# Optimization experiments

Hardware: AMD Instinct MI355X
Metric: run time of the kernel (lower is better)

The kernel has to match this reference:

```python
import jax, jax.numpy as jnp
import numpy as np

NUM_GRAPHS = 16


def gat_layer(x, src, dst, n, W, a_s, a_d, b):
    # PyG GATConv, concat=False (mean over heads), negative_slope=0.2
    H, C = a_s.shape
    h = (x @ W).reshape(x.shape[0], H, C)            # [N,H,C]
    es = jnp.einsum('nhc,hc->nh', h, a_s)            # alpha_src per node
    ed = jnp.einsum('nhc,hc->nh', h, a_d)            # alpha_dst per node
    e = jax.nn.leaky_relu(es[src] + ed[dst], 0.2)    # [E,H]
    m = jax.ops.segment_max(e, dst, num_segments=n)
    m = jnp.where(jnp.isfinite(m), m, 0.0)
    p = jnp.exp(e - m[dst])
    denom = jax.ops.segment_sum(p, dst, num_segments=n)
    alpha = p / (denom[dst] + 1e-16)                 # segment softmax over in-edges
    out = jax.ops.segment_sum(h[src] * alpha[..., None], dst, num_segments=n)  # [N,H,C]
    return out.mean(axis=1) + b


def _forward(x, edge_index, batch,
             W_e0, a_s_e0, a_d_e0, b_e0, W_e1, a_s_e1, a_d_e1, b_e1,
             W_d0, a_s_d0, a_d_d0, b_d0, W_d1, a_s_d1, a_d_d1, b_d1,
             g_w1, g_b1, g_w2, g_b2):
    n = x.shape[0]
    loop = jnp.arange(n, dtype=edge_index.dtype)     # PyG add_self_loops=True
    src = jnp.concatenate([edge_index[0], loop])
    dst = jnp.concatenate([edge_index[1], loop])
    # encoder (dropout inert in eval)
    h = jax.nn.relu(gat_layer(x, src, dst, n, W_e0, a_s_e0, a_d_e0, b_e0))
    h = gat_layer(h, src, dst, n, W_e1, a_s_e1, a_d_e1, b_e1)
    # GlobalAttention pooling: gate MLP -> segment softmax over graphs -> scatter sum
    gate = (jax.nn.relu(h @ g_w1 + g_b1) @ g_w2 + g_b2)[:, 0]   # [N]
    gm = jax.ops.segment_max(gate, batch, num_segments=NUM_GRAPHS)
    gm = jnp.where(jnp.isfinite(gm), gm, 0.0)
    p = jnp.exp(gate - gm[batch])
    att = p / (jax.ops.segment_sum(p, batch, num_segments=NUM_GRAPHS)[batch] + 1e-16)
    pooled = jax.ops.segment_sum(att[:, None] * h, batch, num_segments=NUM_GRAPHS)
    h = pooled[batch]                                # broadcast pooled back to nodes
    # decoder (heads=1)
    h = jax.nn.relu(gat_layer(h, src, dst, n, W_d0, a_s_d0, a_d_d0, b_d0))
    return gat_layer(h, src, dst, n, W_d1, a_s_d1, a_d_d1, b_d1)


def setup_inputs() -> dict:
    key = jax.random.key(0)
    ks = jax.random.split(key, 24)
    N, E, Din, H, C = 50000, 250000, 128, 8, 64
    def w(k, shape, fan_in):
        return (jax.random.normal(k, shape, jnp.float32) / np.sqrt(fan_in)).astype(jnp.float32)
    return {
        'x': jax.random.normal(ks[0], (N, Din), jnp.float32),
        'edge_index': jax.random.randint(ks[1], (2, E), 0, N, dtype=jnp.int32),
        'batch': jnp.sort(jax.random.randint(ks[2], (N,), 0, NUM_GRAPHS, dtype=jnp.int32)),
        'W_e0': w(ks[3], (Din, H * C), Din), 'a_s_e0': w(ks[4], (H, C), C), 'a_d_e0': w(ks[5], (H, C), C), 'b_e0': w(ks[6], (C,), C),
        'W_e1': w(ks[7], (C, H * C), C), 'a_s_e1': w(ks[8], (H, C), C), 'a_d_e1': w(ks[9], (H, C), C), 'b_e1': w(ks[10], (C,), C),
        'W_d0': w(ks[11], (C, C), C), 'a_s_d0': w(ks[12], (1, C), C), 'a_d_d0': w(ks[13], (1, C), C), 'b_d0': w(ks[14], (C,), C),
        'W_d1': w(ks[15], (C, Din), C), 'a_s_d1': w(ks[16], (1, Din), Din), 'a_d_d1': w(ks[17], (1, Din), Din), 'b_d1': w(ks[18], (Din,), Din),
        'g_w1': w(ks[19], (C, C), C), 'g_b1': w(ks[20], (C,), C), 'g_w2': w(ks[21], (C, 1), C), 'g_b2': w(ks[22], (1,), C),
    }


def reference(x, edge_index, batch,
              W_e0, a_s_e0, a_d_e0, b_e0, W_e1, a_s_e1, a_d_e1, b_e1,
              W_d0, a_s_d0, a_d_d0, b_d0, W_d1, a_s_d1, a_d_d1, b_d1,
              g_w1, g_b1, g_w2, g_b2):
    return _forward(x, edge_index, batch,
                    W_e0, a_s_e0, a_d_e0, b_e0, W_e1, a_s_e1, a_d_e1, b_e1,
                    W_d0, a_s_d0, a_d_d0, b_d0, W_d1, a_s_d1, a_d_d1, b_d1,
                    g_w1, g_b1, g_w2, g_b2)
```

## Files before the change

kernel.cpp:

```cpp
#include <hip/hip_runtime.h>
#include <hip/hip_fp16.h>
#include <math.h>

#define TB 256

typedef _Float16 half8v __attribute__((ext_vector_type(8)));
typedef float float4v __attribute__((ext_vector_type(4)));

static __device__ __forceinline__ int edge_src(const int* ei, int E, int e) {
    return (e < E) ? ei[e] : (e - E);
}
static __device__ __forceinline__ int edge_dst(const int* ei, int E, int e) {
    return (e < E) ? ei[E + e] : (e - E);
}

__global__ void csr_count(const int* __restrict__ ei, int E, int Etot, int* __restrict__ cnt) {
    int e = blockIdx.x * blockDim.x + threadIdx.x;
    if (e >= Etot) return;
    atomicAdd(&cnt[edge_dst(ei, E, e)], 1);
}

__global__ __launch_bounds__(256) void scan_phase1(const int* __restrict__ cnt,
                                                   int* __restrict__ incl,
                                                   int* __restrict__ bsum, int n) {
    __shared__ int sdata[256];
    int t = threadIdx.x;
    int base = blockIdx.x * 256;
    int v = (base + t < n) ? cnt[base + t] : 0;
    for (int d = 1; d < 256; d <<= 1) {
        sdata[t] = v; __syncthreads();
        if (t >= d) v += sdata[t - d];
        __syncthreads();
    }
    if (base + t < n) incl[base + t] = v;
    if (t == 255) bsum[blockIdx.x] = v;
}

__global__ void scan_phase2(int* bsum, int nb) {
    __shared__ int sdata[256];
    int t = threadIdx.x;
    int v = (t < nb) ? bsum[t] : 0;
    for (int d = 1; d < 256; d <<= 1) {
        sdata[t] = v; __syncthreads();
        if (t >= d) v += sdata[t - d];
        __syncthreads();
    }
    if (t < nb) bsum[t] = v;
}

__global__ __launch_bounds__(256) void scan_phase3(const int* __restrict__ incl,
                                                   const int* __restrict__ bsum,
                                                   int* __restrict__ off, int n) {
    int i = blockIdx.x * 256 + threadIdx.x;
    if (i < n) off[i + 1] = incl[i] + (blockIdx.x ? bsum[blockIdx.x - 1] : 0);
    if (i == 0) off[0] = 0;
}

__global__ void csr_fill(const int* __restrict__ ei, int E, int Etot,
                         const int* __restrict__ off, int* __restrict__ cur,
                         int* __restrict__ esrc) {
    int e = blockIdx.x * blockDim.x + threadIdx.x;
    if (e >= Etot) return;
    int d = edge_dst(ei, E, e);
    int pos = atomicAdd(&cur[d], 1);
    esrc[off[d] + pos] = edge_src(ei, E, e);
}

__global__ void find_gstart(const int* __restrict__ batch, int* __restrict__ gstart, int N) {
    int n = blockIdx.x * blockDim.x + threadIdx.x;
    if (n >= N) return;
    int b = batch[n];
    int prev = n ? batch[n - 1] : -1;
    for (int g = prev + 1; g <= b; ++g) gstart[g] = n;
    if (n == N - 1)
        for (int g = b + 1; g <= 16; ++g) gstart[g] = N;
}

__global__ void cast_f2h(const float* __restrict__ in, __half* __restrict__ out, int n) {
    int i2 = (blockIdx.x * blockDim.x + threadIdx.x) * 2;
    if (i2 + 1 < n) {
        float2 v = *(const float2*)(in + i2);
        *(__half2*)(out + i2) = __floats2half2_rn(v.x, v.y);
    } else if (i2 < n) {
        out[i2] = __float2half(in[i2]);
    }
}

__global__ void make_ws(const float* __restrict__ W, const float* __restrict__ a_s,
                        const float* __restrict__ a_d, float* __restrict__ ws,
                        float* __restrict__ wd, int K, int H, int C) {
    int i = blockIdx.x * blockDim.x + threadIdx.x;
    if (i >= H * K) return;
    int h = i / K, k = i % K;
    const float* wrow = W + (size_t)k * H * C + h * C;
    float s = 0.f, d = 0.f;
    for (int c = 0; c < C; ++c) {
        s += wrow[c] * a_s[h * C + c];
        d += wrow[c] * a_d[h * C + c];
    }
    ws[i] = s;
    wd[i] = d;
}

__global__ void transpose_cast(const float* __restrict__ W, __half* __restrict__ WT,
                               int K, int N) {
    int i = blockIdx.x * blockDim.x + threadIdx.x;
    if (i >= N * K) return;
    int nn = i / K, kk = i % K;
    WT[i] = __float2half(W[kk * N + nn]);
}

__global__ void make_wstackT(const float* __restrict__ W, __half* __restrict__ WT,
                             int K, int H, int C) {
    int i = blockIdx.x * blockDim.x + threadIdx.x;
    if (i >= K * H * C) return;
    int c = i / (H * K);
    int rem = i % (H * K);
    int h = rem / K, k = rem % K;
    WT[i] = __float2half(W[(size_t)k * H * C + h * C + c]);
}

template <int K>
__global__ __launch_bounds__(256) void gemm_mfma(const __half* __restrict__ A,
                                                 const __half* __restrict__ BT,
                                                 __half* __restrict__ C,
                                                 int M, int N) {
    constexpr int KP = K + 8;
    __shared__ __align__(16) __half As[64 * KP];
    __shared__ __align__(16) __half Bs[64 * KP];
    int tid = threadIdx.x;
    int bm = blockIdx.y * 64, bn = blockIdx.x * 64;
    constexpr int LPR = K / 8;
    for (int idx = tid; idx < 64 * LPR; idx += 256) {
        int row = idx / LPR, koff = (idx % LPR) * 8;
        uint4 v = make_uint4(0u, 0u, 0u, 0u);
        int gr = bm + row;
        if (gr < M) v = *(const uint4*)(A + (size_t)gr * K + koff);
        *(uint4*)(&As[row * KP + koff]) = v;
        uint4 wv = *(const uint4*)(BT + (size_t)(bn + row) * K + koff);
        *(uint4*)(&Bs[row * KP + koff]) = wv;
    }
    __syncthreads();
    int wv_ = tid >> 6, l = tid & 63;
    int lr = l & 15, g = l >> 4;
    float4v acc[4] = {{0.f, 0.f, 0.f, 0.f}, {0.f, 0.f, 0.f, 0.f},
                      {0.f, 0.f, 0.f, 0.f}, {0.f, 0.f, 0.f, 0.f}};
    const __half* ap = &As[(16 * wv_ + lr) * KP + 8 * g];
    const __half* bp = &Bs[lr * KP + 8 * g];
#pragma unroll
    for (int k0 = 0; k0 < K; k0 += 32) {
        half8v af = *reinterpret_cast<const half8v*>(ap + k0);
#pragma unroll
        for (int nt = 0; nt < 4; ++nt) {
            half8v bf = *reinterpret_cast<const half8v*>(bp + nt * 16 * KP + k0);
            acc[nt] = __builtin_amdgcn_mfma_f32_16x16x32_f16(af, bf, acc[nt], 0, 0, 0);
        }
    }
#pragma unroll
    for (int nt = 0; nt < 4; ++nt) {
#pragma unroll
        for (int r = 0; r < 4; ++r) {
            int grow = bm + 16 * wv_ + 4 * g + r;
            if (grow < M)
                C[(size_t)grow * N + bn + nt * 16 + lr] = __float2half(acc[nt][r]);
        }
    }
}

template <int K, int H>
__global__ __launch_bounds__(256) void scores_nt(const __half* __restrict__ A,
                                                 const float* __restrict__ ws,
                                                 const float* __restrict__ wd,
                                                 float* __restrict__ es,
                                                 float* __restrict__ ed, int N) {
    int n = blockIdx.x * blockDim.x + threadIdx.x;
    if (n >= N) return;
    const __half* row = A + (size_t)n * K;
    float s[H] = {}, d[H] = {};
#pragma unroll
    for (int k0 = 0; k0 < K; k0 += 8) {
        uint4 raw = *(const uint4*)(row + k0);
        const __half* hv = (const __half*)&raw;
        float a[8];
#pragma unroll
        for (int q = 0; q < 8; ++q) a[q] = __half2float(hv[q]);
#pragma unroll
        for (int h = 0; h < H; ++h)
#pragma unroll
            for (int q = 0; q < 8; ++q) {
                s[h] += a[q] * ws[h * K + k0 + q];
                d[h] += a[q] * wd[h * K + k0 + q];
            }
    }
#pragma unroll
    for (int h = 0; h < H; ++h) {
        es[(size_t)n * H + h] = s[h];
        ed[(size_t)n * H + h] = d[h];
    }
}

template <bool RELU>
__global__ __launch_bounds__(256) void gat_gather_h8(const __half* __restrict__ hsrc,
                                                     const float* __restrict__ es,
                                                     const float* __restrict__ ed,
                                                     const int* __restrict__ off,
                                                     const int* __restrict__ esrc,
                                                     const float* __restrict__ bias,
                                                     __half* __restrict__ out, int N) {
    constexpr int HC = 512;
    int n = (blockIdx.x * blockDim.x + threadIdx.x) >> 6;
    int lane = threadIdx.x & 63;
    if (n >= N) return;
    int hd = lane >> 3;
    int k8 = lane >> 3, h8 = lane & 7;
    int j0 = off[n], j1 = off[n + 1];

    float edl = ed[(size_t)n * 8 + h8];

    float acc[8] = {};
    float denacc = 0.f;
    for (int j = j0; j < j1; j += 8) {
        int jj = j + k8;
        int jc = (jj < j1) ? jj : (j1 - 1);
        int sidx = esrc[jc];
        float v = es[(size_t)sidx * 8 + h8] + edl;
        v = (v > 0.f) ? v : 0.2f * v;
        float pm = (jj < j1) ? expf(v) : 0.f;
        denacc += pm;
        uint4 rw[8];
#pragma unroll
        for (int k = 0; k < 8; ++k) {
            int sb = __shfl(sidx, k * 8);
            rw[k] = *(const uint4*)(hsrc + (size_t)sb * HC + 8 * lane);
        }
#pragma unroll
        for (int k = 0; k < 8; ++k) {
            float a = __shfl(pm, k * 8 + hd);
            const __half* hv = (const __half*)&rw[k];
#pragma unroll
            for (int q = 0; q < 8; ++q) acc[q] += a * __half2float(hv[q]);
        }
    }

    float den = denacc;
#pragma unroll
    for (int o = 8; o < 64; o <<= 1) den += __shfl_xor(den, o);
    float dv = __shfl(den, hd) + 1e-16f;

#pragma unroll
    for (int q = 0; q < 8; ++q) acc[q] /= dv;
#pragma unroll
    for (int o = 8; o < 64; o <<= 1)
#pragma unroll
        for (int q = 0; q < 8; ++q) acc[q] += __shfl_xor(acc[q], o);

    if (lane < 8) {
        int cbase = 8 * lane;
        float r[8];
#pragma unroll
        for (int q = 0; q < 8; ++q) {
            float o2 = acc[q] * 0.125f + bias[cbase + q];
            if (RELU) o2 = fmaxf(o2, 0.f);
            r[q] = o2;
        }
        __half2 p0 = __floats2half2_rn(r[0], r[1]);
        __half2 p1 = __floats2half2_rn(r[2], r[3]);
        __half2 p2 = __floats2half2_rn(r[4], r[5]);
        __half2 p3 = __floats2half2_rn(r[6], r[7]);
        uint4 pk;
        pk.x = *(unsigned*)&p0; pk.y = *(unsigned*)&p1;
        pk.z = *(unsigned*)&p2; pk.w = *(unsigned*)&p3;
        *(uint4*)(out + (size_t)n * 64 + cbase) = pk;
    }
}

__global__ __launch_bounds__(256) void gat_gather_z8(const __half* __restrict__ A,
                                                     const float* __restrict__ es,
                                                     const float* __restrict__ ed,
                                                     const int* __restrict__ off,
                                                     const int* __restrict__ esrc,
                                                     __half* __restrict__ z, int N) {
    int n = (blockIdx.x * blockDim.x + threadIdx.x) >> 6;
    int lane = threadIdx.x & 63;
    if (n >= N) return;
    int k8 = lane >> 3, q8 = lane & 7;
    int j0 = off[n], j1 = off[n + 1];
    float edv = ed[n];

    float acc[8] = {};
    float denacc = 0.f;
    for (int j = j0; j < j1; j += 8) {
        int jj = j + k8;
        int jc = (jj < j1) ? jj : (j1 - 1);
        int sidx = esrc[jc];
        float v = es[sidx] + edv;
        v = (v > 0.f) ? v : 0.2f * v;
        float pm = (jj < j1) ? expf(v) : 0.f;
        denacc += pm;
        uint4 rw = *(const uint4*)(A + (size_t)sidx * 64 + 8 * q8);
        const __half* hv = (const __half*)&rw;
#pragma unroll
        for (int q = 0; q < 8; ++q) acc[q] += pm * __half2float(hv[q]);
    }

    float den = denacc;
#pragma unroll
    for (int o = 8; o < 64; o <<= 1) {
        den += __shfl_xor(den, o);
#pragma unroll
        for (int q = 0; q < 8; ++q) acc[q] += __shfl_xor(acc[q], o);
    }
    float inv = 1.f / (den + 1e-16f);
    if (lane < 8) {
        float r[8];
#pragma unroll
        for (int q = 0; q < 8; ++q) r[q] = acc[q] * inv;
        __half2 p0 = __floats2half2_rn(r[0], r[1]);
        __half2 p1 = __floats2half2_rn(r[2], r[3]);
        __half2 p2 = __floats2half2_rn(r[4], r[5]);
        __half2 p3 = __floats2half2_rn(r[6], r[7]);
        uint4 pk;
        pk.x = *(unsigned*)&p0; pk.y = *(unsigned*)&p1;
        pk.z = *(unsigned*)&p2; pk.w = *(unsigned*)&p3;
        *(uint4*)(z + (size_t)n * 64 + 8 * lane) = pk;
    }
}

template <int KK, typename OUTT, bool RELU>
__global__ __launch_bounds__(256) void gemm_kt(const __half* __restrict__ A,
                                               const __half* __restrict__ BT,
                                               const float* __restrict__ bias,
                                               OUTT* __restrict__ C,
                                               int M, int Nout) {
    __shared__ __align__(16) __half As[64 * 72];
    __shared__ __align__(16) __half Bs[64 * 72];
    int tid = threadIdx.x;
    int bm = blockIdx.y * 64, bn = blockIdx.x * 64;
    int wv = tid >> 6, l = tid & 63, lr = l & 15, g = l >> 4;
    float4v acc[4] = {{0.f, 0.f, 0.f, 0.f}, {0.f, 0.f, 0.f, 0.f},
                      {0.f, 0.f, 0.f, 0.f}, {0.f, 0.f, 0.f, 0.f}};
    for (int kc = 0; kc < KK; kc += 64) {
        __syncthreads();
        for (int idx = tid; idx < 512; idx += 256) {
            int row = idx >> 3, ko = (idx & 7) * 8;
            uint4 v = make_uint4(0u, 0u, 0u, 0u);
            int gr = bm + row;
            if (gr < M) v = *(const uint4*)(A + (size_t)gr * KK + kc + ko);
            *(uint4*)(&As[row * 72 + ko]) = v;
            uint4 wvv = *(const uint4*)(BT + (size_t)(bn + row) * KK + kc + ko);
            *(uint4*)(&Bs[row * 72 + ko]) = wvv;
        }
        __syncthreads();
#pragma unroll
        for (int k0 = 0; k0 < 64; k0 += 32) {
            half8v af = *reinterpret_cast<const half8v*>(&As[(16 * wv + lr) * 72 + k0 + 8 * g]);
#pragma unroll
            for (int nt = 0; nt < 4; ++nt) {
                half8v bf = *reinterpret_cast<const half8v*>(&Bs[(nt * 16 + lr) * 72 + k0 + 8 * g]);
                acc[nt] = __builtin_amdgcn_mfma_f32_16x16x32_f16(af, bf, acc[nt], 0, 0, 0);
            }
        }
    }
#pragma unroll
    for (int nt = 0; nt < 4; ++nt) {
        float b = bias[bn + nt * 16 + lr];
#pragma unroll
        for (int r = 0; r < 4; ++r) {
            int grow = bm + 16 * wv + 4 * g + r;
            if (grow < M) {
                float c = acc[nt][r] + b;
                if (RELU) c = fmaxf(c, 0.f);
                if constexpr (sizeof(OUTT) == 2)
                    C[(size_t)grow * Nout + bn + nt * 16 + lr] = __float2half(c);
                else
                    C[(size_t)grow * Nout + bn + nt * 16 + lr] = c;
            }
        }
    }
}

__global__ __launch_bounds__(256) void gat_gather_d08(const float* __restrict__ hsrc,
                                                      const float* __restrict__ es16,
                                                      const float* __restrict__ ed16,
                                                      const int* __restrict__ off,
                                                      const int* __restrict__ esrc,
                                                      const int* __restrict__ batch,
                                                      const float* __restrict__ bias,
                                                      __half* __restrict__ out, int N) {
    int n = (blockIdx.x * blockDim.x + threadIdx.x) >> 6;
    int lane = threadIdx.x & 63;
    if (n >= N) return;
    int k8 = lane >> 3, q8 = lane & 7;
    int j0 = off[n], j1 = off[n + 1];
    float edv = ed16[batch[n]];

    float acc[8] = {};
    float denacc = 0.f;
    for (int j = j0; j < j1; j += 8) {
        int jj = j + k8;
        int jc = (jj < j1) ? jj : (j1 - 1);
        int g = batch[esrc[jc]];
        float v = es16[g] + edv;
        v = (v > 0.f) ? v : 0.2f * v;
        float pm = (jj < j1) ? expf(v) : 0.f;
        denacc += pm;
        const float* row = hsrc + (size_t)g * 64 + 8 * q8;
        float4 r0 = *(const float4*)row;
        float4 r1 = *(const float4*)(row + 4);
        acc[0] += pm * r0.x; acc[1] += pm * r0.y;
        acc[2] += pm * r0.z; acc[3] += pm * r0.w;
        acc[4] += pm * r1.x; acc[5] += pm * r1.y;
        acc[6] += pm * r1.z; acc[7] += pm * r1.w;
    }

    float den = denacc;
#pragma unroll
    for (int o = 8; o < 64; o <<= 1) {
        den += __shfl_xor(den, o);
#pragma unroll
        for (int q = 0; q < 8; ++q) acc[q] += __shfl_xor(acc[q], o);
    }
    float inv = 1.f / (den + 1e-16f);
    if (lane < 8) {
        float r[8];
#pragma unroll
        for (int q = 0; q < 8; ++q) r[q] = fmaxf(acc[q] * inv + bias[8 * lane + q], 0.f);
        __half2 p0 = __floats2half2_rn(r[0], r[1]);
        __half2 p1 = __floats2half2_rn(r[2], r[3]);
        __half2 p2 = __floats2half2_rn(r[4], r[5]);
        __half2 p3 = __floats2half2_rn(r[6], r[7]);
        uint4 pk;
        pk.x = *(unsigned*)&p0; pk.y = *(unsigned*)&p1;
        pk.z = *(unsigned*)&p2; pk.w = *(unsigned*)&p3;
        *(uint4*)(out + (size_t)n * 64 + 8 * lane) = pk;
    }
}

__global__ __launch_bounds__(256) void gate_mfma(const __half* __restrict__ A,
                                                 const __half* __restrict__ BT,
                                                 const float* __restrict__ b1,
                                                 const float* __restrict__ w2,
                                                 const float* __restrict__ b2,
                                                 const int* __restrict__ batch,
                                                 float* __restrict__ pg,
                                                 float* __restrict__ gden, int M) {
    constexpr int KP = 72;
    __shared__ __align__(16) __half As[64 * KP];
    __shared__ __align__(16) __half Bs[64 * KP];
    __shared__ float part[16];
    int tid = threadIdx.x;
    if (tid < 16) part[tid] = 0.f;
    int bm = blockIdx.x * 64;
    for (int idx = tid; idx < 512; idx += 256) {
        int row = idx >> 3, ko = (idx & 7) * 8;
        uint4 v = make_uint4(0u, 0u, 0u, 0u);
        int gr = bm + row;
        if (gr < M) v = *(const uint4*)(A + (size_t)gr * 64 + ko);
        *(uint4*)(&As[row * KP + ko]) = v;
        uint4 wvv = *(const uint4*)(BT + (size_t)row * 64 + ko);
        *(uint4*)(&Bs[row * KP + ko]) = wvv;
    }
    __syncthreads();
    int wv_ = tid >> 6, l = tid & 63;
    int lr = l & 15, g = l >> 4;
    float4v acc[4] = {{0.f, 0.f, 0.f, 0.f}, {0.f, 0.f, 0.f, 0.f},
                      {0.f, 0.f, 0.f, 0.f}, {0.f, 0.f, 0.f, 0.f}};
    const __half* ap = &As[(16 * wv_ + lr) * KP + 8 * g];
    const __half* bp = &Bs[lr * KP + 8 * g];
#pragma unroll
    for (int k0 = 0; k0 < 64; k0 += 32) {
        half8v af = *reinterpret_cast<const half8v*>(ap + k0);
#pragma unroll
        for (int nt = 0; nt < 4; ++nt) {
            half8v bf = *reinterpret_cast<const half8v*>(bp + nt * 16 * KP + k0);
            acc[nt] = __builtin_amdgcn_mfma_f32_16x16x32_f16(af, bf, acc[nt], 0, 0, 0);
        }
    }
    float partial[4];
#pragma unroll
    for (int r = 0; r < 4; ++r) {
        float t = 0.f;
#pragma unroll
        for (int nt = 0; nt < 4; ++nt) {
            int col = nt * 16 + lr;
            float tv = acc[nt][r] + b1[col];
            tv = fmaxf(tv, 0.f);
            t += tv * w2[col];
        }
        partial[r] = t;
    }
#pragma unroll
    for (int o = 1; o < 16; o <<= 1)
#pragma unroll
        for (int r = 0; r < 4; ++r) partial[r] += __shfl_xor(partial[r], o);
    if (lr == 0) {
        float bb = b2[0];
#pragma unroll
        for (int r = 0; r < 4; ++r) {
            int grow = bm + 16 * wv_ + 4 * g + r;
            if (grow < M) {
                float p = expf(partial[r] + bb);
                pg[grow] = p;
                atomicAdd(&part[batch[grow]], p);
            }
        }
    }
    __syncthreads();
    if (tid < 16 && part[tid] != 0.f) atomicAdd(&gden[tid], part[tid]);
}

#define POOL_SPLIT 32
__global__ __launch_bounds__(256) void pool_sum2(const __half* __restrict__ h,
                                                 const float* __restrict__ pg,
                                                 const int* __restrict__ gstart,
                                                 float* __restrict__ pooled, int N) {
    __shared__ float part[256];
    int g = blockIdx.x;
    int r0 = gstart[g], r1 = gstart[g + 1];
    int len = r1 - r0;
    int chunk = (len + POOL_SPLIT - 1) / POOL_SPLIT;
    int s0 = r0 + blockIdx.y * chunk;
    int s1 = min(s0 + chunk, r1);
    int wv = threadIdx.x >> 6, lane = threadIdx.x & 63;
    float acc = 0.f;
    for (int n = s0 + wv; n < s1; n += 4)
        acc += pg[n] * __half2float(h[(size_t)n * 64 + lane]);
    part[threadIdx.x] = acc;
    __syncthreads();
    if (threadIdx.x < 64) {
        float tot = part[threadIdx.x] + part[64 + threadIdx.x] +
                    part[128 + threadIdx.x] + part[192 + threadIdx.x];
        if (tot != 0.f) atomicAdd(&pooled[g * 64 + threadIdx.x], tot);
    }
}

__global__ void dec_prep(const float* __restrict__ pooled, const float* __restrict__ gden,
                         const float* __restrict__ Wd0, const float* __restrict__ asd,
                         const float* __restrict__ add, float* __restrict__ hd016,
                         float* __restrict__ es16, float* __restrict__ ed16) {
    int g = blockIdx.x;
    int lane = threadIdx.x;
    float pn = pooled[g * 64 + lane] / (gden[g] + 1e-16f);
    float o = 0.f;
    for (int c = 0; c < 64; ++c) o += __shfl(pn, c) * Wd0[c * 64 + lane];
    hd016[g * 64 + lane] = o;
    float s = o * asd[lane], d = o * add[lane];
#pragma unroll
    for (int off = 32; off; off >>= 1) {
        s += __shfl_xor(s, off);
        d += __shfl_xor(d, off);
    }
    if (lane == 0) {
        es16[g] = s;
        ed16[g] = d;
    }
}

static inline int cdiv(int a, int b) { return (a + b - 1) / b; }

extern "C" void kernel_launch(void* const* d_in, const int* in_sizes, int n_in,
                              void* d_out, int out_size, void* d_ws, size_t ws_size,
                              hipStream_t stream) {
    const float* x      = (const float*)d_in[0];
    const int*   ei     = (const int*)  d_in[1];
    const int*   batch  = (const int*)  d_in[2];
    const float* W_e0   = (const float*)d_in[3];
    const float* a_s_e0 = (const float*)d_in[4];
    const float* a_d_e0 = (const float*)d_in[5];
    const float* b_e0   = (const float*)d_in[6];
    const float* W_e1   = (const float*)d_in[7];
    const float* a_s_e1 = (const float*)d_in[8];
    const float* a_d_e1 = (const float*)d_in[9];
    const float* b_e1   = (const float*)d_in[10];
    const float* W_d0   = (const float*)d_in[11];
    const float* a_s_d0 = (const float*)d_in[12];
    const float* a_d_d0 = (const float*)d_in[13];
    const float* b_d0   = (const float*)d_in[14];
    const float* W_d1   = (const float*)d_in[15];
    const float* a_s_d1 = (const float*)d_in[16];
    const float* a_d_d1 = (const float*)d_in[17];
    const float* b_d1   = (const float*)d_in[18];
    const float* g_w1   = (const float*)d_in[19];
    const float* g_b1   = (const float*)d_in[20];
    const float* g_w2   = (const float*)d_in[21];
    const float* g_b2   = (const float*)d_in[22];

    const int N    = in_sizes[2];
    const int E    = in_sizes[1] / 2;
    const int Etot = E + N;
    const int Din  = in_sizes[0] / N;

    char* w = (char*)d_ws;
    size_t o = 0;
    auto alloc = [&](size_t bytes) -> void* {
        void* p = w + o;
        o = (o + bytes + 255) & ~(size_t)255;
        return p;
    };
    __half*   h16    = (__half*)  alloc((size_t)N * 512 * 2);
    __half*   x16    = (__half*)  alloc((size_t)N * Din * 2);
    __half*   bufA   = (__half*)  alloc((size_t)N * 64 * 2);
    __half*   bufB   = (__half*)  alloc((size_t)N * 64 * 2);
    __half*   wt_e0  = (__half*)  alloc((size_t)512 * 128 * 2);
    __half*   wt_e1  = (__half*)  alloc((size_t)512 * 64 * 2);
    __half*   wst_d1 = (__half*)  alloc((size_t)128 * 64 * 2);
    __half*   wt_g1  = (__half*)  alloc((size_t)64 * 64 * 2);
    float*    ws_e0  = (float*)   alloc(8 * 128 * 4);
    float*    wd_e0  = (float*)   alloc(8 * 128 * 4);
    float*    ws_e1  = (float*)   alloc(8 * 64 * 4);
    float*    wd_e1  = (float*)   alloc(8 * 64 * 4);
    float*    ws_d1  = (float*)   alloc(64 * 4);
    float*    wd_d1  = (float*)   alloc(64 * 4);
    float*    es     = (float*)   alloc((size_t)N * 8 * 4);
    float*    ed     = (float*)   alloc((size_t)N * 8 * 4);
    float*    pg     = (float*)   alloc((size_t)N * 4);
    int*      off    = (int*)     alloc((size_t)(N + 1) * 4);
    int*      cnt    = (int*)     alloc((size_t)N * 4);
    int*      esrc   = (int*)     alloc((size_t)Etot * 4);
    int*      bsum   = (int*)     alloc(256 * 4);
    int*      gstart = (int*)     alloc(17 * 4);
    float*    gden   = (float*)   alloc(16 * 4);
    float*    pooled = (float*)   alloc(16 * 64 * 4);
    float*    hd016  = (float*)   alloc(16 * 64 * 4);
    float*    es16   = (float*)   alloc(16 * 4);
    float*    ed16   = (float*)   alloc(16 * 4);
    (void)ws_size; (void)n_in; (void)out_size;

    const int nodeWaveGrid = cdiv(N, 4);
    const int nodeThreadGrid = cdiv(N, TB);
    const int edgeGrid     = cdiv(Etot, TB);
    const int scanBlocks   = cdiv(N, 256);

    hipMemsetAsync(cnt, 0, (size_t)N * 4, stream);
    csr_count<<<edgeGrid, TB, 0, stream>>>(ei, E, Etot, cnt);
    scan_phase1<<<scanBlocks, 256, 0, stream>>>(cnt, esrc , bsum, N);
    scan_phase2<<<1, 256, 0, stream>>>(bsum, scanBlocks);
    scan_phase3<<<scanBlocks, 256, 0, stream>>>(esrc, bsum, off, N);
    hipMemsetAsync(cnt, 0, (size_t)N * 4, stream);
    csr_fill<<<edgeGrid, TB, 0, stream>>>(ei, E, Etot, off, cnt, esrc);
    find_gstart<<<nodeThreadGrid, TB, 0, stream>>>(batch, gstart, N);

    cast_f2h<<<cdiv(N * Din / 2, TB), TB, 0, stream>>>(x, x16, N * Din);
    transpose_cast<<<cdiv(512 * 128, TB), TB, 0, stream>>>(W_e0, wt_e0, Din, 512);
    transpose_cast<<<cdiv(512 * 64, TB), TB, 0, stream>>>(W_e1, wt_e1, 64, 512);
    transpose_cast<<<cdiv(64 * 64, TB), TB, 0, stream>>>(g_w1, wt_g1, 64, 64);
    make_wstackT<<<cdiv(128 * 64, TB), TB, 0, stream>>>(W_d1, wst_d1, 64, 1, 128);
    make_ws<<<cdiv(8 * 128, TB), TB, 0, stream>>>(W_e0, a_s_e0, a_d_e0, ws_e0, wd_e0, 128, 8, 64);
    make_ws<<<cdiv(8 * 64, TB), TB, 0, stream>>>(W_e1, a_s_e1, a_d_e1, ws_e1, wd_e1, 64, 8, 64);
    make_ws<<<1, TB, 0, stream>>>(W_d1, a_s_d1, a_d_d1, ws_d1, wd_d1, 64, 1, 128);

    scores_nt<128, 8><<<nodeThreadGrid, TB, 0, stream>>>(x16, ws_e0, wd_e0, es, ed, N);
    {
        dim3 grid(512 / 64, cdiv(N, 64));
        gemm_mfma<128><<<grid, TB, 0, stream>>>(x16, wt_e0, h16, N, 512);
    }
    gat_gather_h8<true><<<nodeWaveGrid, TB, 0, stream>>>(
        h16, es, ed, off, esrc, b_e0, bufA, N);

    scores_nt<64, 8><<<nodeThreadGrid, TB, 0, stream>>>(bufA, ws_e1, wd_e1, es, ed, N);
    {
        dim3 grid(512 / 64, cdiv(N, 64));
        gemm_mfma<64><<<grid, TB, 0, stream>>>(bufA, wt_e1, h16, N, 512);
    }
    gat_gather_h8<false><<<nodeWaveGrid, TB, 0, stream>>>(
        h16, es, ed, off, esrc, b_e1, bufB, N);

    hipMemsetAsync(gden, 0, 16 * 4, stream);
    hipMemsetAsync(pooled, 0, 16 * 64 * 4, stream);
    gate_mfma<<<cdiv(N, 64), TB, 0, stream>>>(bufB, wt_g1, g_b1, g_w2, g_b2, batch, pg, gden, N);
    {
        dim3 grid(16, POOL_SPLIT);
        pool_sum2<<<grid, TB, 0, stream>>>(bufB, pg, gstart, pooled, N);
    }
    dec_prep<<<16, 64, 0, stream>>>(pooled, gden, W_d0, a_s_d0, a_d_d0, hd016, es16, ed16);

    gat_gather_d08<<<nodeWaveGrid, TB, 0, stream>>>(
        hd016, es16, ed16, off, esrc, batch, b_d0, bufA, N);

    scores_nt<64, 1><<<nodeThreadGrid, TB, 0, stream>>>(bufA, ws_d1, wd_d1, es, ed, N);
    gat_gather_z8<<<nodeWaveGrid, TB, 0, stream>>>(bufA, es, ed, off, esrc, h16 , N);
    {
        dim3 grid(2, cdiv(N, 64));
        gemm_kt<64, float, false><<<grid, TB, 0, stream>>>(h16 , wst_d1, b_d1, (float*)d_out, N, 128);
    }
}
```

Before: 375.3 us.

## Reorder encoder layer 2 as aggregate-then-project via stacked weight GEMM

For the second encoder GAT layer, the new code first aggregates the 64-wide input features per head with softmax weights into a 512-wide buffer. It then applies one GEMM against the vertically stacked per-head weights, which also folds in the head mean and bias. Previously the 64→512 projection ran first and the gather then read 512-wide rows per edge. The gather now reads 64-wide source rows, which cuts per-edge memory traffic, at the cost of a K=512 GEMM and an extra 512-wide intermediate write. The new gather also drops the max subtraction in the softmax, relying on bounded scores.

```diff
diff --git a/kernel.cpp b/kernel.cpp
--- a/kernel.cpp
+++ b/kernel.cpp
@@ -272,6 +272,64 @@
         pk.z = *(unsigned*)&p2; pk.w = *(unsigned*)&p3;
         *(uint4*)(out + (size_t)n * 64 + cbase) = pk;
     }
+}
+
+__global__ __launch_bounds__(256) void gat_gather_zh8(const __half* __restrict__ A,
+                                                      const float* __restrict__ es,
+                                                      const float* __restrict__ ed,
+                                                      const int* __restrict__ off,
+                                                      const int* __restrict__ esrc,
+                                                      __half* __restrict__ z, int N) {
+    int n = (blockIdx.x * blockDim.x + threadIdx.x) >> 6;
+    int lane = threadIdx.x & 63;
+    if (n >= N) return;
+    int h = lane >> 3, q = lane & 7;
+    int j0 = off[n], j1 = off[n + 1];
+    float edv = ed[(size_t)n * 8 + h];
+
+    float acc[8] = {};
+    float den = 0.f;
+    int j = j0;
+    for (; j + 1 < j1; j += 2) {
+        int s0 = esrc[j], s1 = esrc[j + 1];
+        float v0 = es[(size_t)s0 * 8 + h] + edv;
+        float v1 = es[(size_t)s1 * 8 + h] + edv;
+        v0 = (v0 > 0.f) ? v0 : 0.2f * v0;
+        v1 = (v1 > 0.f) ? v1 : 0.2f * v1;
+        float p0 = expf(v0), p1 = expf(v1);
+        den += p0 + p1;
+        uint4 r0 = *(const uint4*)(A + (size_t)s0 * 64 + 8 * q);
+        uint4 r1 = *(const uint4*)(A + (size_t)s1 * 64 + 8 * q);
+        const __half* h0 = (const __half*)&r0;
+        const __half* h1 = (const __half*)&r1;
+#pragma unroll
+        for (int k = 0; k < 8; ++k)
+            acc[k] += p0 * __half2float(h0[k]) + p1 * __half2float(h1[k]);
+    }
+    if (j < j1) {
+        int s0 = esrc[j];
+        float v0 = es[(size_t)s0 * 8 + h] + edv;
+        v0 = (v0 > 0.f) ? v0 : 0.2f * v0;
+        float p0 = expf(v0);
+        den += p0;
+        uint4 r0 = *(const uint4*)(A + (size_t)s0 * 64 + 8 * q);
+        const __half* h0 = (const __half*)&r0;
+#pragma unroll
+        for (int k = 0; k < 8; ++k) acc[k] += p0 * __half2float(h0[k]);
+    }
+
+    float inv = 1.f / ((den + 1e-16f) * 8.f);
+    float r[8];
+#pragma unroll
+    for (int k = 0; k < 8; ++k) r[k] = acc[k] * inv;
+    __half2 p0 = __floats2half2_rn(r[0], r[1]);
+    __half2 p1 = __floats2half2_rn(r[2], r[3]);
+    __half2 p2 = __floats2half2_rn(r[4], r[5]);
+    __half2 p3 = __floats2half2_rn(r[6], r[7]);
+    uint4 pk;
+    pk.x = *(unsigned*)&p0; pk.y = *(unsigned*)&p1;
+    pk.z = *(unsigned*)&p2; pk.w = *(unsigned*)&p3;
+    *(uint4*)(z + (size_t)n * 512 + h * 64 + 8 * q) = pk;
 }
 
 __global__ __launch_bounds__(256) void gat_gather_z8(const __half* __restrict__ A,
@@ -602,7 +660,7 @@
     __half*   bufA   = (__half*)  alloc((size_t)N * 64 * 2);
     __half*   bufB   = (__half*)  alloc((size_t)N * 64 * 2);
     __half*   wt_e0  = (__half*)  alloc((size_t)512 * 128 * 2);
-    __half*   wt_e1  = (__half*)  alloc((size_t)512 * 64 * 2);
+    __half*   wst_e1 = (__half*)  alloc((size_t)64 * 512 * 2);
     __half*   wst_d1 = (__half*)  alloc((size_t)128 * 64 * 2);
     __half*   wt_g1  = (__half*)  alloc((size_t)64 * 64 * 2);
     float*    ws_e0  = (float*)   alloc(8 * 128 * 4);
@@ -642,8 +700,8 @@
 
     cast_f2h<<<cdiv(N * Din / 2, TB), TB, 0, stream>>>(x, x16, N * Din);
     transpose_cast<<<cdiv(512 * 128, TB), TB, 0, stream>>>(W_e0, wt_e0, Din, 512);
-    transpose_cast<<<cdiv(512 * 64, TB), TB, 0, stream>>>(W_e1, wt_e1, 64, 512);
     transpose_cast<<<cdiv(64 * 64, TB), TB, 0, stream>>>(g_w1, wt_g1, 64, 64);
+    make_wstackT<<<cdiv(64 * 512, TB), TB, 0, stream>>>(W_e1, wst_e1, 64, 8, 64);
     make_wstackT<<<cdiv(128 * 64, TB), TB, 0, stream>>>(W_d1, wst_d1, 64, 1, 128);
     make_ws<<<cdiv(8 * 128, TB), TB, 0, stream>>>(W_e0, a_s_e0, a_d_e0, ws_e0, wd_e0, 128, 8, 64);
     make_ws<<<cdiv(8 * 64, TB), TB, 0, stream>>>(W_e1, a_s_e1, a_d_e1, ws_e1, wd_e1, 64, 8, 64);
@@ -658,12 +716,11 @@
         h16, es, ed, off, esrc, b_e0, bufA, N);
 
     scores_nt<64, 8><<<nodeThreadGrid, TB, 0, stream>>>(bufA, ws_e1, wd_e1, es, ed, N);
+    gat_gather_zh8<<<nodeWaveGrid, TB, 0, stream>>>(bufA, es, ed, off, esrc, h16 , N);
     {
-        dim3 grid(512 / 64, cdiv(N, 64));
-        gemm_mfma<64><<<grid, TB, 0, stream>>>(bufA, wt_e1, h16, N, 512);
-    }
-    gat_gather_h8<false><<<nodeWaveGrid, TB, 0, stream>>>(
-        h16, es, ed, off, esrc, b_e1, bufB, N);
+        dim3 grid(1, cdiv(N, 64));
+        gemm_kt<512, __half, false><<<grid, TB, 0, stream>>>(h16 , wst_e1, b_e1, bufB, N, 64);
+    }
 
     hipMemsetAsync(gden, 0, 16 * 4, stream);
     hipMemsetAsync(pooled, 0, 16 * 64 * 4, stream);
```

Result: faster. 352.6 us (-6.0%).
